# Kernel tuning notes

Measured on AMD Instinct MI355X. Metric: run time of the kernel, lower is better.

Reference implementation:

```python
import jax, jax.numpy as jnp
import numpy as np

B, F, H, L, K = 16384, 1024, 1024, 256, 7

def _lin(key, fi, fo, lead=()):
    k1, k2 = jax.random.split(key)
    s = 1.0 / np.sqrt(fi)
    W = jax.random.uniform(k1, lead + (fi, fo), jnp.float32, -s, s)
    b = jax.random.uniform(k2, lead + (fo,), jnp.float32, -s, s)
    return W, b

def setup_inputs() -> dict:
    ks = jax.random.split(jax.random.key(0), 16)
    x = jax.random.normal(ks[0], (B, F), jnp.float32)
    t = jax.random.randint(ks[1], (B,), 0, K, jnp.int32)
    y = jax.random.normal(ks[2], (B,), jnp.float32)
    d = jax.random.normal(ks[3], (B,), jnp.float32)
    tw0, tb0 = _lin(ks[4], F, L)
    tw1, tb1 = _lin(ks[5], L, L)
    tw2, tb2 = _lin(ks[6], L, K)
    yw0, yb0 = _lin(ks[7], F, H)
    yw1, yb1 = _lin(ks[8], H, H)
    yhW, yhb = _lin(ks[9], H, 2, (K,))
    dw0, db0 = _lin(ks[10], F, H)
    dw1, db1 = _lin(ks[11], H, H)
    dhW, dhb = _lin(ks[12], H, 2, (K,))
    zw0, zb0 = _lin(ks[13], F + 2, H)
    zw1, zb1 = _lin(ks[14], H, H)
    zhW, zhb = _lin(ks[15], H, 2 * L, (K,))
    return dict(x=x, t=t, y=y, d=d, tw0=tw0, tb0=tb0, tw1=tw1, tb1=tb1, tw2=tw2, tb2=tb2,
                yw0=yw0, yb0=yb0, yw1=yw1, yb1=yb1, yhW=yhW, yhb=yhb,
                dw0=dw0, db0=db0, dw1=dw1, db1=db1, dhW=dhW, dhb=dhb,
                zw0=zw0, zb0=zb0, zw1=zw1, zb1=zb1, zhW=zhW, zhb=zhb)

def _mlp2(x, w0, b0, w1, b1):
    # FullyConnected([in, H, H], final_activation=ELU)
    return jax.nn.elu(jax.nn.elu(x @ w0 + b0) @ w1 + b1)

def _select(hidden, t, hW, hb):
    # dense compute of all K treatment heads, then per-row gather by t
    all_out = jnp.einsum('bh,khd->bkd', hidden, hW) + hb  # [B, K, D]
    return jnp.take_along_axis(all_out, t[:, None, None], axis=1)[:, 0]

def _normal_head(sel):
    # pyro NormalNet head on a scalar outcome
    loc = jnp.clip(sel[:, 0:1], -1e6, 1e6)
    scale = jnp.minimum(jax.nn.softplus(sel[:, 1:2]) + 1e-3, 1e6)
    return loc, scale

def _diagnormal_head(sel):
    loc = jnp.clip(sel[:, :L], -100.0, 100.0)
    scale = jnp.minimum(jax.nn.softplus(sel[:, L:]) + 0.001, 100.0)
    return loc, scale

def reference(x, t, y, d, tw0, tb0, tw1, tb1, tw2, tb2,
              yw0, yb0, yw1, yb1, yhW, yhb,
              dw0, db0, dw1, db1, dhW, dhb,
              zw0, zb0, zw1, zb1, zhW, zhb):
    # t_nn: MultinormNet, ELU final activation then clamp(-10, 10)
    t_logits = jnp.clip(jax.nn.elu(_mlp2(x, tw0, tb0, tw1, tb1) @ tw2 + tb2), -10.0, 10.0)
    # y_dist(t, x)
    hy = _mlp2(x, yw0, yb0, yw1, yb1)
    y_loc, y_scale = _normal_head(_select(hy, t, yhW, yhb))
    # d_dist(t, x)
    hd = _mlp2(x, dw0, db0, dw1, db1)
    d_loc, d_scale = _normal_head(_select(hd, t, dhW, dhb))
    # z_dist(y, d, t, x): hidden from cat([y, d, x])
    hz = _mlp2(jnp.concatenate([y[:, None], d[:, None], x], axis=-1), zw0, zb0, zw1, zb1)
    z_loc, z_scale = _diagnormal_head(_select(hz, t, zhW, zhb))
    # [B, K + 4 + 2L]
    return jnp.concatenate([t_logits, y_loc, y_scale, d_loc, d_scale, z_loc, z_scale], axis=-1)
```

## Files before the change

### kernel.cpp

```cpp
#include <hip/hip_runtime.h>
#include <hip/hip_bf16.h>
#include <cstdint>
#include <cstddef>

typedef __hip_bfloat16 bf16;
typedef __bf16 bf16x8 __attribute__((ext_vector_type(8)));
typedef float f32x4 __attribute__((ext_vector_type(4)));

#define DEVFN static __device__ __forceinline__

DEVFN void async16(const void* g, void* l) {
  __builtin_amdgcn_global_load_lds(
      (const __attribute__((address_space(1))) uint32_t*)g,
      (__attribute__((address_space(3))) uint32_t*)l, 16, 0, 0);
}

DEVFN float eluf(float v) { return v > 0.f ? v : expm1f(v); }
DEVFN float softplusf(float x) {
  return x > 0.f ? x + log1pf(expf(-x)) : log1pf(expf(x));
}

DEVFN void nt_store_bf16(float v, bf16* p) {
  bf16 h = __float2bfloat16(v);
  unsigned short u;
  __builtin_memcpy(&u, &h, 2);
  __builtin_nontemporal_store(u, (unsigned short*)p);
}

template <int NCHB, int NFB>
DEVFN void kloop64(const bf16* (&gA)[4], const bf16* (&gB)[NCHB], bf16* As,
                   bf16* Bs, int tid, const bf16* aBase, const bf16* bBase,
                   const int (&colsel)[2], f32x4 (&acc)[4][NFB], int kiters) {
  for (int kt = 0; kt < kiters; ++kt) {
#pragma unroll
    for (int c = 0; c < 4; ++c) async16(gA[c], As + c * 2048 + tid * 8);
#pragma unroll
    for (int c = 0; c < NCHB; ++c) async16(gB[c], Bs + c * 2048 + tid * 8);
#pragma unroll
    for (int c = 0; c < 4; ++c) gA[c] += 64;
#pragma unroll
    for (int c = 0; c < NCHB; ++c) gB[c] += 64;
    __syncthreads();
#pragma unroll
    for (int s = 0; s < 2; ++s) {
      bf16x8 af[4], bfv[NFB];
#pragma unroll
      for (int r = 0; r < 4; ++r)
        af[r] = *(const bf16x8*)(aBase + r * 1024 + colsel[s]);
#pragma unroll
      for (int c = 0; c < NFB; ++c)
        bfv[c] = *(const bf16x8*)(bBase + c * 1024 + colsel[s]);
#pragma unroll
      for (int r = 0; r < 4; ++r)
#pragma unroll
        for (int c = 0; c < NFB; ++c)
          acc[r][c] = __builtin_amdgcn_mfma_f32_16x16x32_bf16(af[r], bfv[c], acc[r][c], 0, 0, 0);
    }
    __syncthreads();
  }
}

DEVFN void transpose_tile(const float* src, bf16* dst, int R, int C, int bx, int by) {
  __shared__ float tile[32][33];
  const int c0 = bx * 32, r0 = by * 32;
  const int tx = threadIdx.x & 31, ty = threadIdx.x >> 5;
#pragma unroll
  for (int rr = ty; rr < 32; rr += 8)
    tile[rr][tx] = src[(size_t)(r0 + rr) * C + c0 + tx];
  __syncthreads();
#pragma unroll
  for (int rr = ty; rr < 32; rr += 8)
    dst[(size_t)(c0 + rr) * R + r0 + tx] = __float2bfloat16(tile[tx][rr]);
}

__global__ __launch_bounds__(256) void prep_all_k(
    const float* __restrict__ x, bf16* __restrict__ xb,
    const float* __restrict__ yw0, const float* __restrict__ dw0,
    const float* __restrict__ zw0, const float* __restrict__ tw0,
    bf16* __restrict__ BtL1,
    const float* __restrict__ yw1, const float* __restrict__ dw1,
    const float* __restrict__ zw1, bf16* __restrict__ BtL2,
    const float* __restrict__ tw1, bf16* __restrict__ tw1t,
    const float* __restrict__ zhW, bf16* __restrict__ zhWt,
    const float* __restrict__ yb0, const float* __restrict__ db0,
    const float* __restrict__ zb0, const float* __restrict__ tb0,
    const float* __restrict__ yb1, const float* __restrict__ db1,
    const float* __restrict__ zb1,
    float* __restrict__ biasAll, float* __restrict__ r0All,
    float* __restrict__ r1All, float* __restrict__ biasL2,
    const int* __restrict__ t, int* __restrict__ cnt, int* __restrict__ seg,
    int* __restrict__ rank, int* __restrict__ sids) {
  int l = blockIdx.x;
  if (l < 8192) {
    size_t i = ((size_t)l * 256 + threadIdx.x) * 8;
    float4 v0 = *(const float4*)(x + i);
    float4 v1 = *(const float4*)(x + i + 4);
    union { bf16 h[8]; uint4 u; } o;
    o.h[0] = __float2bfloat16(v0.x); o.h[1] = __float2bfloat16(v0.y);
    o.h[2] = __float2bfloat16(v0.z); o.h[3] = __float2bfloat16(v0.w);
    o.h[4] = __float2bfloat16(v1.x); o.h[5] = __float2bfloat16(v1.y);
    o.h[6] = __float2bfloat16(v1.z); o.h[7] = __float2bfloat16(v1.w);
    *(uint4*)(xb + i) = o.u;
    return;
  }
  l -= 8192;
  if (l < 4096) {
    int z = l >> 10, rem = l & 1023, bx = rem & 31, by = rem >> 5;
    const float* src = (z == 0) ? yw0 : (z == 1) ? dw0 : (z == 2) ? zw0 + 2048 : tw0;
    int C = (z == 3) ? 256 : 1024;
    if (bx * 32 < C)
      transpose_tile(src, BtL1 + (size_t)z * 1024 * 1024, 1024, C, bx, by);
    return;
  }
  l -= 4096;
  if (l < 3072) {
    int z = l >> 10, rem = l & 1023, bx = rem & 31, by = rem >> 5;
    const float* src = (z == 0) ? yw1 : (z == 1) ? dw1 : zw1;
    transpose_tile(src, BtL2 + (size_t)z * 1024 * 1024, 1024, 1024, bx, by);
    return;
  }
  l -= 3072;
  if (l < 64) {
    transpose_tile(tw1, tw1t, 256, 256, l & 7, l >> 3);
    return;
  }
  l -= 64;
  if (l < 3584) {
    int z = l >> 9, rem = l & 511, bx = rem & 15, by = rem >> 4;
    transpose_tile(zhW + (size_t)z * 1024 * 512, zhWt + (size_t)z * 512 * 1024,
                   1024, 512, bx, by);
    return;
  }
  l -= 3584;
  if (l < 13) {
    int i = l * 256 + threadIdx.x;
    if (i >= 3328) return;
    float b;
    if (i < 1024) b = yb0[i];
    else if (i < 2048) b = db0[i - 1024];
    else if (i < 3072) b = zb0[i - 2048];
    else b = tb0[i - 3072];
    biasAll[i] = b;
    bool inz = (i >= 2048 && i < 3072);
    r0All[i] = inz ? zw0[i - 2048] : 0.f;
    r1All[i] = inz ? zw0[1024 + (i - 2048)] : 0.f;
    if (i < 3072)
      biasL2[i] = (i < 1024) ? yb1[i] : (i < 2048) ? db1[i - 1024] : zb1[i - 2048];
    return;
  }
  {
    __shared__ int h[8], sseg[8];
    const int tid = threadIdx.x;
    if (tid < 8) h[tid] = 0;
    __syncthreads();
    const int base = tid * 64;
    int lc[7] = {0, 0, 0, 0, 0, 0, 0};
    for (int i = 0; i < 64; ++i) lc[t[base + i]]++;
    int myoff[7];
#pragma unroll
    for (int k = 0; k < 7; ++k) myoff[k] = atomicAdd(&h[k], lc[k]);
    __syncthreads();
    if (tid == 0) {
      int s = 0;
      for (int k = 0; k < 7; ++k) { sseg[k] = s; s += h[k]; }
      sseg[7] = s;
    }
    __syncthreads();
    if (tid < 7) { cnt[tid] = h[tid]; seg[tid] = sseg[tid]; }
    if (tid == 7) seg[7] = sseg[7];
    int cur[7];
#pragma unroll
    for (int k = 0; k < 7; ++k) cur[k] = sseg[k] + myoff[k];
    for (int i = 0; i < 64; ++i) {
      int b = base + i, k = t[b];
      int r = cur[k]++;
      rank[b] = r;
      sids[r] = b;
    }
  }
}

__global__ __launch_bounds__(256) void gemm_l1_k(
    const bf16* __restrict__ A, const bf16* __restrict__ Bt,
    const float* __restrict__ biasAll, const float* __restrict__ r0All,
    const float* __restrict__ r1All, const float* __restrict__ yv,
    const float* __restrict__ dv, bf16* __restrict__ a1y,
    bf16* __restrict__ a1d, bf16* __restrict__ a1z, bf16* __restrict__ ht1) {
  __shared__ bf16 As[128 * 64];
  __shared__ bf16 Bs[128 * 64];
  const int tid = threadIdx.x, lane = tid & 63, wid = tid >> 6;
  const int wm = wid >> 1, wn = wid & 1, quad = lane >> 4, l15 = lane & 15;
  const int id = blockIdx.x;
  const int xcd = id & 7, lid = id >> 3;
  const int pass = lid / 208, rem = lid - pass * 208;
  const int mt = xcd * 16 + pass * 8 + (rem & 7), nt = rem >> 3;
  const int bm0 = mt * 128, bn0 = nt * 128;
  const int sr3 = tid >> 3, scol = ((tid & 7) ^ (sr3 & 7)) * 8;
  const bf16* gA[4];
  const bf16* gB[4];
#pragma unroll
  for (int c = 0; c < 4; ++c) {
    gA[c] = A + (size_t)(bm0 + c * 32 + sr3) * 1024 + scol;
    gB[c] = Bt + (size_t)(bn0 + c * 32 + sr3) * 1024 + scol;
  }
  const bf16* aBase = &As[(wm * 64 + l15) * 64];
  const bf16* bBase = &Bs[(wn * 64 + l15) * 64];
  int colsel[2];
#pragma unroll
  for (int s = 0; s < 2; ++s) colsel[s] = ((s * 4 + quad) ^ (l15 & 7)) * 8;
  f32x4 acc[4][4] = {};
  kloop64<4, 4>(gA, gB, As, Bs, tid, aBase, bBase, colsel, acc, 16);

  const int g = nt >> 3;
  bf16* dst = (g == 0) ? a1y : (g == 1) ? a1d : (g == 2) ? a1z : ht1;
  const int ldc = (g == 3) ? 256 : 1024;
  const int colb = bn0 - g * 1024;
  float bv[4], z0[4], z1[4];
#pragma unroll
  for (int c = 0; c < 4; ++c) {
    int gn = bn0 + wn * 64 + c * 16 + l15;
    bv[c] = biasAll[gn]; z0[c] = r0All[gn]; z1[c] = r1All[gn];
  }
#pragma unroll
  for (int r = 0; r < 4; ++r) {
#pragma unroll
    for (int q = 0; q < 4; ++q) {
      int gm = bm0 + wm * 64 + r * 16 + quad * 4 + q;
      float yy = yv[gm], dd = dv[gm];
#pragma unroll
      for (int c = 0; c < 4; ++c) {
        float v = acc[r][c][q] + bv[c] + yy * z0[c] + dd * z1[c];
        nt_store_bf16(eluf(v), dst + (size_t)gm * ldc + colb + wn * 64 + c * 16 + l15);
      }
    }
  }
}

__global__ __launch_bounds__(256) void gemm_l2t_k(
    const bf16* __restrict__ a1y, const bf16* __restrict__ a1d,
    const bf16* __restrict__ a1z, const bf16* __restrict__ ht1,
    const bf16* __restrict__ BtL2, const bf16* __restrict__ tw1t,
    const float* __restrict__ biasL2, const float* __restrict__ tb1,
    bf16* __restrict__ hyd, bf16* __restrict__ hzg, bf16* __restrict__ ht2,
    const int* __restrict__ rank) {
  __shared__ bf16 As[128 * 64];
  __shared__ bf16 Bs[128 * 64];
  const int tid = threadIdx.x, lane = tid & 63, wid = tid >> 6;
  const int wm = wid >> 1, wn = wid & 1, quad = lane >> 4, l15 = lane & 15;
  const int id = blockIdx.x;
  int bm0, bn0, Ka, g;
  const bf16 *Aptr, *Bptr;
  if (id < 3072) {
    const int xcd = id & 7, lid = id >> 3;
    const int pass = lid / 192, rem = lid - pass * 192;
    const int mt = xcd * 16 + pass * 8 + (rem & 7), nt = rem >> 3;
    bm0 = mt * 128; bn0 = nt * 128; Ka = 1024;
    g = nt >> 3;
    Aptr = (g == 0) ? a1y : (g == 1) ? a1d : a1z;
    Bptr = BtL2;
  } else {
    const int local = id - 3072;
    bm0 = (local >> 1) * 128; bn0 = (local & 1) * 128; Ka = 256;
    g = 3; Aptr = ht1; Bptr = tw1t;
  }
  const int sr3 = tid >> 3, scol = ((tid & 7) ^ (sr3 & 7)) * 8;
  const bf16* gA[4];
  const bf16* gB[4];
#pragma unroll
  for (int c = 0; c < 4; ++c) {
    gA[c] = Aptr + (size_t)(bm0 + c * 32 + sr3) * Ka + scol;
    gB[c] = Bptr + (size_t)(bn0 + c * 32 + sr3) * Ka + scol;
  }
  const bf16* aBase = &As[(wm * 64 + l15) * 64];
  const bf16* bBase = &Bs[(wn * 64 + l15) * 64];
  int colsel[2];
#pragma unroll
  for (int s = 0; s < 2; ++s) colsel[s] = ((s * 4 + quad) ^ (l15 & 7)) * 8;
  f32x4 acc[4][4] = {};
  kloop64<4, 4>(gA, gB, As, Bs, tid, aBase, bBase, colsel, acc, Ka >> 6);

  const float* bias = (g == 3) ? tb1 : biasL2;
  float bv[4];
#pragma unroll
  for (int c = 0; c < 4; ++c) bv[c] = bias[bn0 + wn * 64 + c * 16 + l15];
#pragma unroll
  for (int r = 0; r < 4; ++r) {
#pragma unroll
    for (int q = 0; q < 4; ++q) {
      int gm = bm0 + wm * 64 + r * 16 + quad * 4 + q;
      bf16* dst; size_t rowoff;
      if (g == 2) { dst = hzg; rowoff = (size_t)rank[gm] * 1024 + (size_t)(bn0 - 2048); }
      else if (g == 3) { dst = ht2; rowoff = (size_t)gm * 256 + bn0; }
      else { dst = hyd; rowoff = (size_t)gm * 2048 + bn0; }
#pragma unroll
      for (int c = 0; c < 4; ++c) {
        float v = acc[r][c][q] + bv[c];
        nt_store_bf16(eluf(v), dst + rowoff + wn * 64 + c * 16 + l15);
      }
    }
  }
}

#define ZMT 28
#define ZB (7 * ZMT * 8)
__global__ __launch_bounds__(256) void tail_k(
    const bf16* __restrict__ hzg, const bf16* __restrict__ zhWt,
    const float* __restrict__ zhb, const int* __restrict__ seg,
    const int* __restrict__ cnts, const int* __restrict__ sids,
    const bf16* __restrict__ hyd, const bf16* __restrict__ ht2,
    const int* __restrict__ t, const float* __restrict__ yhW,
    const float* __restrict__ yhb, const float* __restrict__ dhW,
    const float* __restrict__ dhb, const float* __restrict__ tw2,
    const float* __restrict__ tb2, float* __restrict__ out) {
  __shared__ bf16 As[128 * 64];
  __shared__ bf16 Bs[64 * 64];
  const int tid = threadIdx.x, lane = tid & 63, wid = tid >> 6;
  const int wv = wid, quad = lane >> 4, l15 = lane & 15;
  if (blockIdx.x < ZB) {
    const int kb = blockIdx.x / (ZMT * 8);
    const int r = blockIdx.x % (ZMT * 8);
    const int cnt = cnts[kb];
    const int bm0 = (r >> 3) * 128;
    if (bm0 >= cnt) return;
    const int n0 = (r & 7) * 64;
    const int wm = wid >> 1, wn = wid & 1;
    const int base = seg[kb];
    const int sr3 = tid >> 3, scol = ((tid & 7) ^ (sr3 & 7)) * 8;
    const bf16* gA[4];
    const bf16* gB[2];
#pragma unroll
    for (int c = 0; c < 4; ++c) {
      int rr = bm0 + c * 32 + sr3;
      if (rr >= cnt) rr = cnt - 1;
      gA[c] = hzg + (size_t)(base + rr) * 1024 + scol;
    }
#pragma unroll
    for (int c = 0; c < 2; ++c)
      gB[c] = zhWt + (size_t)kb * 512 * 1024 + (size_t)(n0 + c * 32 + sr3) * 1024 + scol;
    const bf16* aBase = &As[(wm * 64 + l15) * 64];
    const bf16* bBase = &Bs[(wn * 32 + l15) * 64];
    int colsel[2];
#pragma unroll
    for (int s = 0; s < 2; ++s) colsel[s] = ((s * 4 + quad) ^ (l15 & 7)) * 8;
    f32x4 acc[4][2] = {};
    kloop64<2, 2>(gA, gB, As, Bs, tid, aBase, bBase, colsel, acc, 16);
    const float* bias = zhb + (size_t)kb * 512;
    float bv[2]; int gnn[2];
#pragma unroll
    for (int c = 0; c < 2; ++c) {
      gnn[c] = n0 + wn * 32 + c * 16 + l15;
      bv[c] = bias[gnn[c]];
    }
#pragma unroll
    for (int r2 = 0; r2 < 4; ++r2)
#pragma unroll
      for (int q = 0; q < 4; ++q) {
        int lm = bm0 + wm * 64 + r2 * 16 + quad * 4 + q;
        if (lm < cnt) {
          int gm = sids[base + lm];
          size_t ob = (size_t)gm * 523 + 11;
#pragma unroll
          for (int c = 0; c < 2; ++c) {
            float v = acc[r2][c][q] + bv[c];
            int n = gnn[c];
            float o = (n < 256) ? fminf(fmaxf(v, -100.f), 100.f)
                                : fminf(softplusf(v) + 0.001f, 100.f);
            __builtin_nontemporal_store(o, out + ob + n);
          }
        }
      }
    return;
  }
  const int hid = blockIdx.x - ZB;
  if (hid < 4096) {
    const int b = hid * 4 + wv;
    const int tb = t[b];
    const float* yW = yhW + (size_t)tb * 2048;
    const float* dW = dhW + (size_t)tb * 2048;
    float s0 = 0.f, s1 = 0.f, s2 = 0.f, s3 = 0.f;
    for (int i = lane; i < 1024; i += 64) {
      float a = __bfloat162float(hyd[(size_t)b * 2048 + i]);
      float c = __bfloat162float(hyd[(size_t)b * 2048 + 1024 + i]);
      s0 += a * yW[2 * i]; s1 += a * yW[2 * i + 1];
      s2 += c * dW[2 * i]; s3 += c * dW[2 * i + 1];
    }
#pragma unroll
    for (int off = 32; off > 0; off >>= 1) {
      s0 += __shfl_down(s0, off); s1 += __shfl_down(s1, off);
      s2 += __shfl_down(s2, off); s3 += __shfl_down(s3, off);
    }
    if (lane == 0) {
      size_t o = (size_t)b * 523;
      __builtin_nontemporal_store(fminf(fmaxf(s0 + yhb[tb * 2], -1e6f), 1e6f), out + o + 7);
      __builtin_nontemporal_store(fminf(softplusf(s1 + yhb[tb * 2 + 1]) + 1e-3f, 1e6f), out + o + 8);
      __builtin_nontemporal_store(fminf(fmaxf(s2 + dhb[tb * 2], -1e6f), 1e6f), out + o + 9);
      __builtin_nontemporal_store(fminf(softplusf(s3 + dhb[tb * 2 + 1]) + 1e-3f, 1e6f), out + o + 10);
    }
  } else {
    const int b = (hid - 4096) * 4 + wv;
    float h[4];
#pragma unroll
    for (int j = 0; j < 4; ++j)
      h[j] = __bfloat162float(ht2[(size_t)b * 256 + lane * 4 + j]);
    float pp[7];
#pragma unroll
    for (int kk = 0; kk < 7; ++kk) {
      float s = 0.f;
#pragma unroll
      for (int j = 0; j < 4; ++j) s += h[j] * tw2[(lane * 4 + j) * 7 + kk];
      pp[kk] = s;
    }
#pragma unroll
    for (int kk = 0; kk < 7; ++kk)
#pragma unroll
      for (int off = 32; off > 0; off >>= 1) pp[kk] += __shfl_down(pp[kk], off);
    if (lane == 0) {
#pragma unroll
      for (int kk = 0; kk < 7; ++kk) {
        float v = eluf(pp[kk] + tb2[kk]);
        __builtin_nontemporal_store(fminf(fmaxf(v, -10.f), 10.f), out + (size_t)b * 523 + kk);
      }
    }
  }
}

extern "C" void kernel_launch(void* const* d_in, const int* in_sizes, int n_in,
                              void* d_out, int out_size, void* d_ws, size_t ws_size,
                              hipStream_t stream) {
  const float* x   = (const float*)d_in[0];
  const int*   t   = (const int*)d_in[1];
  const float* yv  = (const float*)d_in[2];
  const float* dv  = (const float*)d_in[3];
  const float* tw0 = (const float*)d_in[4];
  const float* tb0 = (const float*)d_in[5];
  const float* tw1 = (const float*)d_in[6];
  const float* tb1 = (const float*)d_in[7];
  const float* tw2 = (const float*)d_in[8];
  const float* tb2 = (const float*)d_in[9];
  const float* yw0 = (const float*)d_in[10];
  const float* yb0 = (const float*)d_in[11];
  const float* yw1 = (const float*)d_in[12];
  const float* yb1 = (const float*)d_in[13];
  const float* yhW = (const float*)d_in[14];
  const float* yhb = (const float*)d_in[15];
  const float* dw0 = (const float*)d_in[16];
  const float* db0 = (const float*)d_in[17];
  const float* dw1 = (const float*)d_in[18];
  const float* db1 = (const float*)d_in[19];
  const float* dhW = (const float*)d_in[20];
  const float* dhb = (const float*)d_in[21];
  const float* zw0 = (const float*)d_in[22];
  const float* zb0 = (const float*)d_in[23];
  const float* zw1 = (const float*)d_in[24];
  const float* zb1 = (const float*)d_in[25];
  const float* zhW = (const float*)d_in[26];
  const float* zhb = (const float*)d_in[27];
  float* out = (float*)d_out;

  const int B = 16384;
  char* p = (char*)d_ws;
  auto take = [&](size_t bytes) {
    char* r = p;
    p += (bytes + 255) & ~(size_t)255;
    return r;
  };
  bf16*  BtL1    = (bf16*)take((size_t)3328 * 1024 * 2);
  bf16*  BtL2    = (bf16*)take((size_t)3072 * 1024 * 2);
  bf16*  tw1t    = (bf16*)take((size_t)256 * 256 * 2);
  bf16*  zhWt    = (bf16*)take((size_t)7 * 512 * 1024 * 2);
  float* biasAll = (float*)take(3328 * 4);
  float* r0All   = (float*)take(3328 * 4);
  float* r1All   = (float*)take(3328 * 4);
  float* biasL2  = (float*)take(3072 * 4);
  int*   cnt     = (int*)take(8 * 4);
  int*   seg     = (int*)take(8 * 4);
  int*   rank    = (int*)take((size_t)B * 4);
  int*   sids    = (int*)take((size_t)B * 4);
  bf16*  xb      = (bf16*)take((size_t)B * 1024 * 2);
  bf16*  a1y     = (bf16*)take((size_t)B * 1024 * 2);
  bf16*  a1d     = (bf16*)take((size_t)B * 1024 * 2);
  bf16*  a1z     = (bf16*)take((size_t)B * 1024 * 2);
  bf16*  ht1     = (bf16*)take((size_t)B * 256 * 2);
  bf16*  hyd     = (bf16*)take((size_t)B * 2048 * 2);
  bf16*  ht2     = (bf16*)take((size_t)B * 256 * 2);
  bf16*  hzg     = xb;

  prep_all_k<<<19022, 256, 0, stream>>>(x, xb, yw0, dw0, zw0, tw0, BtL1,
                                        yw1, dw1, zw1, BtL2, tw1, tw1t, zhW, zhWt,
                                        yb0, db0, zb0, tb0, yb1, db1, zb1,
                                        biasAll, r0All, r1All, biasL2,
                                        t, cnt, seg, rank, sids);
  gemm_l1_k<<<3328, 256, 0, stream>>>(xb, BtL1, biasAll, r0All, r1All,
                                      yv, dv, a1y, a1d, a1z, ht1);
  gemm_l2t_k<<<3328, 256, 0, stream>>>(a1y, a1d, a1z, ht1, BtL2, tw1t,
                                       biasL2, tb1, hyd, hzg, ht2, rank);
  tail_k<<<ZB + 8192, 256, 0, stream>>>(hzg, zhWt, zhb, seg, cnt, sids,
                                        hyd, ht2, t, yhW, yhb, dhW, dhb,
                                        tw2, tb2, out);
}
```

Measured before the change: 744.1 us.

## Halve GEMM K-tile to 32 with new LDS swizzle and drop nontemporal stores

Changes the shared GEMM main loop from a 64-wide to a 32-wide K step, halving LDS tiles and adjusting the XOR swizzle and load mapping to match. This doubles the number of sync-separated iterations in every GEMM kernel. Smaller LDS footprint may let more blocks fit per CU. Separately, all nontemporal stores for intermediates and outputs become ordinary stores, so intermediate activations can stay in cache for the following kernels.

```diff
diff --git a/kernel.cpp b/kernel.cpp
--- a/kernel.cpp
+++ b/kernel.cpp
@@ -20,45 +20,36 @@
   return x > 0.f ? x + log1pf(expf(-x)) : log1pf(expf(x));
 }
 
-DEVFN void nt_store_bf16(float v, bf16* p) {
-  bf16 h = __float2bfloat16(v);
-  unsigned short u;
-  __builtin_memcpy(&u, &h, 2);
-  __builtin_nontemporal_store(u, (unsigned short*)p);
-}
-
-template <int NCHB, int NFB>
-DEVFN void kloop64(const bf16* (&gA)[4], const bf16* (&gB)[NCHB], bf16* As,
+template <int NAH, int NBH, int NFB>
+DEVFN void kloop32(const bf16* (&gA)[NAH], const bf16* (&gB)[NBH], bf16* As,
                    bf16* Bs, int tid, const bf16* aBase, const bf16* bBase,
-                   const int (&colsel)[2], f32x4 (&acc)[4][NFB], int kiters) {
+                   int colsel, f32x4 (&acc)[4][NFB], int kiters) {
   for (int kt = 0; kt < kiters; ++kt) {
 #pragma unroll
-    for (int c = 0; c < 4; ++c) async16(gA[c], As + c * 2048 + tid * 8);
-#pragma unroll
-    for (int c = 0; c < NCHB; ++c) async16(gB[c], Bs + c * 2048 + tid * 8);
-#pragma unroll
-    for (int c = 0; c < 4; ++c) gA[c] += 64;
-#pragma unroll
-    for (int c = 0; c < NCHB; ++c) gB[c] += 64;
+    for (int c = 0; c < NAH; ++c) async16(gA[c], As + c * 2048 + tid * 8);
+#pragma unroll
+    for (int c = 0; c < NBH; ++c) async16(gB[c], Bs + c * 2048 + tid * 8);
+#pragma unroll
+    for (int c = 0; c < NAH; ++c) gA[c] += 32;
+#pragma unroll
+    for (int c = 0; c < NBH; ++c) gB[c] += 32;
     __syncthreads();
-#pragma unroll
-    for (int s = 0; s < 2; ++s) {
-      bf16x8 af[4], bfv[NFB];
-#pragma unroll
-      for (int r = 0; r < 4; ++r)
-        af[r] = *(const bf16x8*)(aBase + r * 1024 + colsel[s]);
+    bf16x8 af[4], bfv[NFB];
+#pragma unroll
+    for (int r = 0; r < 4; ++r) af[r] = *(const bf16x8*)(aBase + r * 512 + colsel);
+#pragma unroll
+    for (int c = 0; c < NFB; ++c) bfv[c] = *(const bf16x8*)(bBase + c * 512 + colsel);
+#pragma unroll
+    for (int r = 0; r < 4; ++r)
 #pragma unroll
       for (int c = 0; c < NFB; ++c)
-        bfv[c] = *(const bf16x8*)(bBase + c * 1024 + colsel[s]);
-#pragma unroll
-      for (int r = 0; r < 4; ++r)
-#pragma unroll
-        for (int c = 0; c < NFB; ++c)
-          acc[r][c] = __builtin_amdgcn_mfma_f32_16x16x32_bf16(af[r], bfv[c], acc[r][c], 0, 0, 0);
-    }
+        acc[r][c] = __builtin_amdgcn_mfma_f32_16x16x32_bf16(af[r], bfv[c], acc[r][c], 0, 0, 0);
     __syncthreads();
   }
 }
+
+DEVFN int swz_scol(int tid) { return (((tid & 3) ^ ((tid >> 3) & 3)) * 8); }
+DEVFN int swz_colsel(int quad, int l15) { return ((quad ^ ((l15 >> 1) & 3)) * 8); }
 
 DEVFN void transpose_tile(const float* src, bf16* dst, int R, int C, int bx, int by) {
   __shared__ float tile[32][33];
@@ -186,8 +177,8 @@
     const float* __restrict__ r1All, const float* __restrict__ yv,
     const float* __restrict__ dv, bf16* __restrict__ a1y,
     bf16* __restrict__ a1d, bf16* __restrict__ a1z, bf16* __restrict__ ht1) {
-  __shared__ bf16 As[128 * 64];
-  __shared__ bf16 Bs[128 * 64];
+  __shared__ bf16 As[128 * 32];
+  __shared__ bf16 Bs[128 * 32];
   const int tid = threadIdx.x, lane = tid & 63, wid = tid >> 6;
   const int wm = wid >> 1, wn = wid & 1, quad = lane >> 4, l15 = lane & 15;
   const int id = blockIdx.x;
@@ -195,21 +186,19 @@
   const int pass = lid / 208, rem = lid - pass * 208;
   const int mt = xcd * 16 + pass * 8 + (rem & 7), nt = rem >> 3;
   const int bm0 = mt * 128, bn0 = nt * 128;
-  const int sr3 = tid >> 3, scol = ((tid & 7) ^ (sr3 & 7)) * 8;
-  const bf16* gA[4];
-  const bf16* gB[4];
-#pragma unroll
-  for (int c = 0; c < 4; ++c) {
-    gA[c] = A + (size_t)(bm0 + c * 32 + sr3) * 1024 + scol;
-    gB[c] = Bt + (size_t)(bn0 + c * 32 + sr3) * 1024 + scol;
-  }
-  const bf16* aBase = &As[(wm * 64 + l15) * 64];
-  const bf16* bBase = &Bs[(wn * 64 + l15) * 64];
-  int colsel[2];
-#pragma unroll
-  for (int s = 0; s < 2; ++s) colsel[s] = ((s * 4 + quad) ^ (l15 & 7)) * 8;
+  const int sr = tid >> 2, scol = swz_scol(tid);
+  const bf16* gA[2];
+  const bf16* gB[2];
+#pragma unroll
+  for (int c = 0; c < 2; ++c) {
+    gA[c] = A + (size_t)(bm0 + c * 64 + sr) * 1024 + scol;
+    gB[c] = Bt + (size_t)(bn0 + c * 64 + sr) * 1024 + scol;
+  }
+  const bf16* aBase = &As[(wm * 64 + l15) * 32];
+  const bf16* bBase = &Bs[(wn * 64 + l15) * 32];
+  const int colsel = swz_colsel(quad, l15);
   f32x4 acc[4][4] = {};
-  kloop64<4, 4>(gA, gB, As, Bs, tid, aBase, bBase, colsel, acc, 16);
+  kloop32<2, 2, 4>(gA, gB, As, Bs, tid, aBase, bBase, colsel, acc, 32);
 
   const int g = nt >> 3;
   bf16* dst = (g == 0) ? a1y : (g == 1) ? a1d : (g == 2) ? a1z : ht1;
@@ -230,7 +219,7 @@
 #pragma unroll
       for (int c = 0; c < 4; ++c) {
         float v = acc[r][c][q] + bv[c] + yy * z0[c] + dd * z1[c];
-        nt_store_bf16(eluf(v), dst + (size_t)gm * ldc + colb + wn * 64 + c * 16 + l15);
+        dst[(size_t)gm * ldc + colb + wn * 64 + c * 16 + l15] = __float2bfloat16(eluf(v));
       }
     }
   }
@@ -243,8 +232,8 @@
     const float* __restrict__ biasL2, const float* __restrict__ tb1,
     bf16* __restrict__ hyd, bf16* __restrict__ hzg, bf16* __restrict__ ht2,
     const int* __restrict__ rank) {
-  __shared__ bf16 As[128 * 64];
-  __shared__ bf16 Bs[128 * 64];
+  __shared__ bf16 As[128 * 32];
+  __shared__ bf16 Bs[128 * 32];
   const int tid = threadIdx.x, lane = tid & 63, wid = tid >> 6;
   const int wm = wid >> 1, wn = wid & 1, quad = lane >> 4, l15 = lane & 15;
   const int id = blockIdx.x;
@@ -263,21 +252,19 @@
     bm0 = (local >> 1) * 128; bn0 = (local & 1) * 128; Ka = 256;
     g = 3; Aptr = ht1; Bptr = tw1t;
   }
-  const int sr3 = tid >> 3, scol = ((tid & 7) ^ (sr3 & 7)) * 8;
-  const bf16* gA[4];
-  const bf16* gB[4];
-#pragma unroll
-  for (int c = 0; c < 4; ++c) {
-    gA[c] = Aptr + (size_t)(bm0 + c * 32 + sr3) * Ka + scol;
-    gB[c] = Bptr + (size_t)(bn0 + c * 32 + sr3) * Ka + scol;
-  }
-  const bf16* aBase = &As[(wm * 64 + l15) * 64];
-  const bf16* bBase = &Bs[(wn * 64 + l15) * 64];
-  int colsel[2];
-#pragma unroll
-  for (int s = 0; s < 2; ++s) colsel[s] = ((s * 4 + quad) ^ (l15 & 7)) * 8;
+  const int sr = tid >> 2, scol = swz_scol(tid);
+  const bf16* gA[2];
+  const bf16* gB[2];
+#pragma unroll
+  for (int c = 0; c < 2; ++c) {
+    gA[c] = Aptr + (size_t)(bm0 + c * 64 + sr) * Ka + scol;
+    gB[c] = Bptr + (size_t)(bn0 + c * 64 + sr) * Ka + scol;
+  }
+  const bf16* aBase = &As[(wm * 64 + l15) * 32];
+  const bf16* bBase = &Bs[(wn * 64 + l15) * 32];
+  const int colsel = swz_colsel(quad, l15);
   f32x4 acc[4][4] = {};
-  kloop64<4, 4>(gA, gB, As, Bs, tid, aBase, bBase, colsel, acc, Ka >> 6);
+  kloop32<2, 2, 4>(gA, gB, As, Bs, tid, aBase, bBase, colsel, acc, Ka >> 5);
 
   const float* bias = (g == 3) ? tb1 : biasL2;
   float bv[4];
@@ -295,7 +282,7 @@
 #pragma unroll
       for (int c = 0; c < 4; ++c) {
         float v = acc[r][c][q] + bv[c];
-        nt_store_bf16(eluf(v), dst + rowoff + wn * 64 + c * 16 + l15);
+        dst[rowoff + wn * 64 + c * 16 + l15] = __float2bfloat16(eluf(v));
       }
     }
   }
@@ -312,8 +299,8 @@
     const float* __restrict__ yhb, const float* __restrict__ dhW,
     const float* __restrict__ dhb, const float* __restrict__ tw2,
     const float* __restrict__ tb2, float* __restrict__ out) {
-  __shared__ bf16 As[128 * 64];
-  __shared__ bf16 Bs[64 * 64];
+  __shared__ bf16 As[128 * 32];
+  __shared__ bf16 Bs[64 * 32];
   const int tid = threadIdx.x, lane = tid & 63, wid = tid >> 6;
   const int wv = wid, quad = lane >> 4, l15 = lane & 15;
   if (blockIdx.x < ZB) {
@@ -325,25 +312,21 @@
     const int n0 = (r & 7) * 64;
     const int wm = wid >> 1, wn = wid & 1;
     const int base = seg[kb];
-    const int sr3 = tid >> 3, scol = ((tid & 7) ^ (sr3 & 7)) * 8;
-    const bf16* gA[4];
-    const bf16* gB[2];
-#pragma unroll
-    for (int c = 0; c < 4; ++c) {
-      int rr = bm0 + c * 32 + sr3;
+    const int sr = tid >> 2, scol = swz_scol(tid);
+    const bf16* gA[2];
+    const bf16* gB[1];
+#pragma unroll
+    for (int c = 0; c < 2; ++c) {
+      int rr = bm0 + c * 64 + sr;
       if (rr >= cnt) rr = cnt - 1;
       gA[c] = hzg + (size_t)(base + rr) * 1024 + scol;
     }
-#pragma unroll
-    for (int c = 0; c < 2; ++c)
-      gB[c] = zhWt + (size_t)kb * 512 * 1024 + (size_t)(n0 + c * 32 + sr3) * 1024 + scol;
-    const bf16* aBase = &As[(wm * 64 + l15) * 64];
-    const bf16* bBase = &Bs[(wn * 32 + l15) * 64];
-    int colsel[2];
-#pragma unroll
-    for (int s = 0; s < 2; ++s) colsel[s] = ((s * 4 + quad) ^ (l15 & 7)) * 8;
+    gB[0] = zhWt + (size_t)kb * 512 * 1024 + (size_t)(n0 + sr) * 1024 + scol;
+    const bf16* aBase = &As[(wm * 64 + l15) * 32];
+    const bf16* bBase = &Bs[(wn * 32 + l15) * 32];
+    const int colsel = swz_colsel(quad, l15);
     f32x4 acc[4][2] = {};
-    kloop64<2, 2>(gA, gB, As, Bs, tid, aBase, bBase, colsel, acc, 16);
+    kloop32<2, 1, 2>(gA, gB, As, Bs, tid, aBase, bBase, colsel, acc, 32);
     const float* bias = zhb + (size_t)kb * 512;
     float bv[2]; int gnn[2];
 #pragma unroll
@@ -363,9 +346,8 @@
           for (int c = 0; c < 2; ++c) {
             float v = acc[r2][c][q] + bv[c];
             int n = gnn[c];
-            float o = (n < 256) ? fminf(fmaxf(v, -100.f), 100.f)
-                                : fminf(softplusf(v) + 0.001f, 100.f);
-            __builtin_nontemporal_store(o, out + ob + n);
+            out[ob + n] = (n < 256) ? fminf(fmaxf(v, -100.f), 100.f)
+                                    : fminf(softplusf(v) + 0.001f, 100.f);
           }
         }
       }
@@ -391,10 +373,10 @@
     }
     if (lane == 0) {
       size_t o = (size_t)b * 523;
-      __builtin_nontemporal_store(fminf(fmaxf(s0 + yhb[tb * 2], -1e6f), 1e6f), out + o + 7);
-      __builtin_nontemporal_store(fminf(softplusf(s1 + yhb[tb * 2 + 1]) + 1e-3f, 1e6f), out + o + 8);
-      __builtin_nontemporal_store(fminf(fmaxf(s2 + dhb[tb * 2], -1e6f), 1e6f), out + o + 9);
-      __builtin_nontemporal_store(fminf(softplusf(s3 + dhb[tb * 2 + 1]) + 1e-3f, 1e6f), out + o + 10);
+      out[o + 7] = fminf(fmaxf(s0 + yhb[tb * 2], -1e6f), 1e6f);
+      out[o + 8] = fminf(softplusf(s1 + yhb[tb * 2 + 1]) + 1e-3f, 1e6f);
+      out[o + 9] = fminf(fmaxf(s2 + dhb[tb * 2], -1e6f), 1e6f);
+      out[o + 10] = fminf(softplusf(s3 + dhb[tb * 2 + 1]) + 1e-3f, 1e6f);
     }
   } else {
     const int b = (hid - 4096) * 4 + wv;
@@ -418,7 +400,7 @@
 #pragma unroll
       for (int kk = 0; kk < 7; ++kk) {
         float v = eluf(pp[kk] + tb2[kk]);
-        __builtin_nontemporal_store(fminf(fmaxf(v, -10.f), 10.f), out + (size_t)b * 523 + kk);
+        out[(size_t)b * 523 + kk] = fminf(fmaxf(v, -10.f), 10.f);
       }
     }
   }
```

New measurement: 661.8 us. -11.1%, faster.
